# Kernel tuning notes

Hardware: AMD Instinct MI355X
Metric: run time of the kernel (lower is better)

Reference implementation:

```python
import jax, jax.numpy as jnp
from jax import lax
import numpy as np

HIDDEN_DIM = 64
INPUT_DIM = 1
NUM_CLASSES = 3
B, T = 2048, 512


def _lstm_layer(x_tbd, w_ih, w_hh, b_ih, b_hh):
    # x_tbd: [T, B, D_in]; PyTorch gate order: i, f, g, o
    H = w_hh.shape[1]
    bsz = x_tbd.shape[1]
    # precompute input projections for all timesteps: [T, B, 4H]
    xp = jnp.einsum('tbd,gd->tbg', x_tbd, w_ih) + b_ih + b_hh

    def step(carry, xg):
        h, c = carry
        gates = xg + h @ w_hh.T  # [B, 4H]
        i, f, g, o = jnp.split(gates, 4, axis=-1)
        i = jax.nn.sigmoid(i)
        f = jax.nn.sigmoid(f)
        g = jnp.tanh(g)
        o = jax.nn.sigmoid(o)
        c = f * c + i * g
        h = o * jnp.tanh(c)
        return (h, c), h

    h0 = jnp.zeros((bsz, H), dtype=x_tbd.dtype)
    c0 = jnp.zeros((bsz, H), dtype=x_tbd.dtype)
    (h_last, _), ys = lax.scan(step, (h0, c0), xp)
    return ys, h_last


def setup_inputs() -> dict:
    key = jax.random.key(0)
    ks = jax.random.split(key, 12)
    s_in = 1.0 / np.sqrt(HIDDEN_DIM)
    H4 = 4 * HIDDEN_DIM
    return {
        'x': jax.random.normal(ks[0], (B, T, INPUT_DIM), dtype=jnp.float32),
        'w_ih0': jax.random.uniform(ks[1], (H4, INPUT_DIM), minval=-s_in, maxval=s_in),
        'w_hh0': jax.random.uniform(ks[2], (H4, HIDDEN_DIM), minval=-s_in, maxval=s_in),
        'b_ih0': jax.random.uniform(ks[3], (H4,), minval=-s_in, maxval=s_in),
        'b_hh0': jax.random.uniform(ks[4], (H4,), minval=-s_in, maxval=s_in),
        'w_ih1': jax.random.uniform(ks[5], (H4, HIDDEN_DIM), minval=-s_in, maxval=s_in),
        'w_hh1': jax.random.uniform(ks[6], (H4, HIDDEN_DIM), minval=-s_in, maxval=s_in),
        'b_ih1': jax.random.uniform(ks[7], (H4,), minval=-s_in, maxval=s_in),
        'b_hh1': jax.random.uniform(ks[8], (H4,), minval=-s_in, maxval=s_in),
        'w_fc': jax.random.uniform(ks[9], (NUM_CLASSES, HIDDEN_DIM), minval=-s_in, maxval=s_in),
        'b_fc': jax.random.uniform(ks[10], (NUM_CLASSES,), minval=-s_in, maxval=s_in),
    }


def reference(x, w_ih0, w_hh0, b_ih0, b_hh0, w_ih1, w_hh1, b_ih1, b_hh1, w_fc, b_fc):
    # eval-mode forward (dropout between layers disabled)
    x_tbd = jnp.transpose(x, (1, 0, 2))  # [T, B, 1]
    ys0, _ = _lstm_layer(x_tbd, w_ih0, w_hh0, b_ih0, b_hh0)  # [T, B, H]
    _, h_last = _lstm_layer(ys0, w_ih1, w_hh1, b_ih1, b_hh1)  # [B, H]
    return h_last @ w_fc.T + b_fc  # [B, NUM_CLASSES]
```

## Files before the change

### kernel.cpp

```cpp
#include <hip/hip_runtime.h>


typedef _Float16 half8    __attribute__((ext_vector_type(8)));
typedef float    float4_t __attribute__((ext_vector_type(4)));
typedef float    float2_t __attribute__((ext_vector_type(2)));

#define T_STEPS 512
#define SIG_K  (-1.442695040888963f)
#define TANH_K (-2.885390081777927f)

__device__ __forceinline__ int hoff(int slot, int row, int kb, int lo) {
    return slot * 1024 + row * 64 + (((kb + row) & 7) << 3) + lo;
}

__device__ __forceinline__ float lstm_cell(float zi, float zf, float zg, float zo,
                                           float& c) {
    const float ei = __builtin_amdgcn_exp2f(zi);
    const float ef = __builtin_amdgcn_exp2f(zf);
    const float v  = __builtin_amdgcn_exp2f(zg);
    const float eo = __builtin_amdgcn_exp2f(zo);
    const float pi = 1.f + ei, pf = 1.f + ef, pv = 1.f + v, po = 1.f + eo;
    const float A   = pi * pv;
    const float num = fmaf(c, A, (1.f - v) * pf);
    const float cn  = num * __builtin_amdgcn_rcpf(pf * A);
    c = cn;
    const float u = __builtin_amdgcn_exp2f(cn * TANH_K);
    return (1.f - u) * __builtin_amdgcn_rcpf(po * (1.f + u));
}

extern "C" __global__ __launch_bounds__(512, 1)
void lstm2_mfma(const float* __restrict__ x,
                const float* __restrict__ w_ih0, const float* __restrict__ w_hh0,
                const float* __restrict__ b_ih0, const float* __restrict__ b_hh0,
                const float* __restrict__ w_ih1, const float* __restrict__ w_hh1,
                const float* __restrict__ b_ih1, const float* __restrict__ b_hh1,
                const float* __restrict__ w_fc,  const float* __restrict__ b_fc,
                float* __restrict__ out)
{
    __shared__ float    x_lds[T_STEPS][8];
    __shared__ _Float16 bufA[2 * 1024];
    __shared__ _Float16 bufB[2 * 1024];
    __shared__ float    hfin[8][68];

    const int tid  = threadIdx.x;
    const int wv   = tid >> 6;
    const int lane = tid & 63;
    const int cr   = lane & 15;
    const int kg   = lane >> 4;
    const int rb   = kg * 4;
    const int b0   = blockIdx.x * 8;
    const bool isL0 = (wv < 4);
    const int u    = wv & 3;
    const int ucol = u * 16 + cr;
    const int wkb  = 2 * u + (cr >> 3);

    for (int idx = tid; idx < 8 * T_STEPS; idx += 512) {
        const int r = idx >> 9, t = idx & (T_STEPS - 1);
        x_lds[t][r] = x[(long)(b0 + r) * T_STEPS + t];
    }
    for (int idx = tid; idx < 2 * 1024; idx += 512) {
        bufA[idx] = (_Float16)0.f;
        bufB[idx] = (_Float16)0.f;
    }

    half8 wf[4][4];
    float bias[4], wi0[4];
    #pragma unroll
    for (int g = 0; g < 4; ++g) {
        const float sc = (g == 2) ? TANH_K : SIG_K;
        const int col = g * 64 + ucol;
        if (isL0) {
            bias[g] = (b_ih0[col] + b_hh0[col]) * sc;
            wi0[g]  = w_ih0[col] * sc;
            #pragma unroll
            for (int kt = 0; kt < 2; ++kt) {
                const float* src = w_hh0 + col * 64 + kt * 32 + kg * 8;
                #pragma unroll
                for (int i = 0; i < 8; ++i) wf[g][kt][i] = (_Float16)(src[i] * sc);
            }
        } else {
            bias[g] = (b_ih1[col] + b_hh1[col]) * sc;
            #pragma unroll
            for (int kt = 0; kt < 4; ++kt) {
                const int k0 = kt * 32 + kg * 8;
                const float* src = (k0 < 64) ? (w_ih1 + col * 64 + k0)
                                             : (w_hh1 + col * 64 + (k0 - 64));
                #pragma unroll
                for (int i = 0; i < 8; ++i) wf[g][kt][i] = (_Float16)(src[i] * sc);
            }
        }
    }

    const float4_t zero4 = {0.f, 0.f, 0.f, 0.f};
    float cc[2] = {0.f, 0.f};
    float hv[2] = {0.f, 0.f};

    __syncthreads();

    for (int k = 0; k <= T_STEPS; ++k) {
        const int sA = (k + 1) & 1;

        if (isL0) {
            if (k < T_STEPS) {
                const half8 a0 = *(const half8*)&bufA[hoff(sA, cr, kg,     0)];
                const half8 a1 = *(const half8*)&bufA[hoff(sA, cr, 4 + kg, 0)];
                float4_t acc[4];
                #pragma unroll
                for (int g = 0; g < 4; ++g) {
                    acc[g] = __builtin_amdgcn_mfma_f32_16x16x32_f16(a0, wf[g][0], zero4, 0, 0, 0);
                    acc[g] = __builtin_amdgcn_mfma_f32_16x16x32_f16(a1, wf[g][1], acc[g], 0, 0, 0);
                }
                const float2_t xq = *(const float2_t*)&x_lds[k][2 * kg];
                #pragma unroll
                for (int ii = 0; ii < 2; ++ii) {
                    const float xv = xq[ii];
                    const float zi = fmaf(xv, wi0[0], acc[0][ii] + bias[0]);
                    const float zf = fmaf(xv, wi0[1], acc[1][ii] + bias[1]);
                    const float zg = fmaf(xv, wi0[2], acc[2][ii] + bias[2]);
                    const float zo = fmaf(xv, wi0[3], acc[3][ii] + bias[3]);
                    const float h = lstm_cell(zi, zf, zg, zo, cc[ii]);
                    bufA[hoff(k & 1, rb + ii, wkb, cr & 7)] = (_Float16)h;
                }
            }
        } else {
            if (k >= 1) {
                const int sB = k & 1;
                const half8 a0  = *(const half8*)&bufA[hoff(sA, cr, kg,     0)];
                const half8 a1  = *(const half8*)&bufA[hoff(sA, cr, 4 + kg, 0)];
                const half8 bh0 = *(const half8*)&bufB[hoff(sB, cr, kg,     0)];
                const half8 bh1 = *(const half8*)&bufB[hoff(sB, cr, 4 + kg, 0)];
                float4_t acc[4];
                #pragma unroll
                for (int g = 0; g < 4; ++g) {
                    acc[g] = __builtin_amdgcn_mfma_f32_16x16x32_f16(a0,  wf[g][0], zero4, 0, 0, 0);
                    acc[g] = __builtin_amdgcn_mfma_f32_16x16x32_f16(a1,  wf[g][1], acc[g], 0, 0, 0);
                    acc[g] = __builtin_amdgcn_mfma_f32_16x16x32_f16(bh0, wf[g][2], acc[g], 0, 0, 0);
                    acc[g] = __builtin_amdgcn_mfma_f32_16x16x32_f16(bh1, wf[g][3], acc[g], 0, 0, 0);
                }
                #pragma unroll
                for (int ii = 0; ii < 2; ++ii) {
                    const float zi = acc[0][ii] + bias[0];
                    const float zf = acc[1][ii] + bias[1];
                    const float zg = acc[2][ii] + bias[2];
                    const float zo = acc[3][ii] + bias[3];
                    hv[ii] = lstm_cell(zi, zf, zg, zo, cc[ii]);
                    bufB[hoff((k + 1) & 1, rb + ii, wkb, cr & 7)] = (_Float16)hv[ii];
                }
            }
        }

        __syncthreads();
    }

    if (!isL0) {
        hfin[2 * kg + 0][ucol] = hv[0];
        hfin[2 * kg + 1][ucol] = hv[1];
    }
    __syncthreads();

    if (tid < 24) {
        const int row = tid / 3, cls = tid - row * 3;
        float s = b_fc[cls];
        const float* wr = w_fc + cls * 64;
        #pragma unroll 8
        for (int uu = 0; uu < 64; ++uu) s += hfin[row][uu] * wr[uu];
        out[(long)(b0 + row) * 3 + cls] = s;
    }
}

extern "C" void kernel_launch(void* const* d_in, const int* in_sizes, int n_in,
                              void* d_out, int out_size, void* d_ws, size_t ws_size,
                              hipStream_t stream) {
    const float* xx     = (const float*)d_in[0];
    const float* w_ih0  = (const float*)d_in[1];
    const float* w_hh0  = (const float*)d_in[2];
    const float* b_ih0  = (const float*)d_in[3];
    const float* b_hh0  = (const float*)d_in[4];
    const float* w_ih1  = (const float*)d_in[5];
    const float* w_hh1  = (const float*)d_in[6];
    const float* b_ih1  = (const float*)d_in[7];
    const float* b_hh1  = (const float*)d_in[8];
    const float* w_fc   = (const float*)d_in[9];
    const float* b_fc   = (const float*)d_in[10];
    float* out = (float*)d_out;

    lstm2_mfma<<<dim3(256), dim3(512), 0, stream>>>(
        xx, w_ih0, w_hh0, b_ih0, b_hh0,
        w_ih1, w_hh1, b_ih1, b_hh1, w_fc, b_fc, out);
}
```

Measured before the change: 268.7 us.

## Halve batch rows per block and double grid to 512 blocks

Each block now processes 4 batch rows instead of 8, and the grid doubles to 512 blocks. Each lane computes one LSTM cell per step instead of two, which shortens the serial per-step critical path. Launch bounds are raised to allow up to 4 blocks per CU, so more blocks can share a CU and hide latency. The MFMA work per step is unchanged while half the output rows are discarded, so matrix-unit efficiency halves and total MFMA issue doubles.

```diff
diff --git a/kernel.cpp b/kernel.cpp
--- a/kernel.cpp
+++ b/kernel.cpp
@@ -3,7 +3,6 @@
 
 typedef _Float16 half8    __attribute__((ext_vector_type(8)));
 typedef float    float4_t __attribute__((ext_vector_type(4)));
-typedef float    float2_t __attribute__((ext_vector_type(2)));
 
 #define T_STEPS 512
 #define SIG_K  (-1.442695040888963f)
@@ -28,7 +27,7 @@
     return (1.f - u) * __builtin_amdgcn_rcpf(po * (1.f + u));
 }
 
-extern "C" __global__ __launch_bounds__(512, 1)
+extern "C" __global__ __launch_bounds__(512, 4)
 void lstm2_mfma(const float* __restrict__ x,
                 const float* __restrict__ w_ih0, const float* __restrict__ w_hh0,
                 const float* __restrict__ b_ih0, const float* __restrict__ b_hh0,
@@ -37,10 +36,10 @@
                 const float* __restrict__ w_fc,  const float* __restrict__ b_fc,
                 float* __restrict__ out)
 {
-    __shared__ float    x_lds[T_STEPS][8];
+    __shared__ float    x_lds[T_STEPS][4];
     __shared__ _Float16 bufA[2 * 1024];
     __shared__ _Float16 bufB[2 * 1024];
-    __shared__ float    hfin[8][68];
+    __shared__ float    hfin[4][68];
 
     const int tid  = threadIdx.x;
     const int wv   = tid >> 6;
@@ -48,13 +47,13 @@
     const int cr   = lane & 15;
     const int kg   = lane >> 4;
     const int rb   = kg * 4;
-    const int b0   = blockIdx.x * 8;
+    const int b0   = blockIdx.x * 4;
     const bool isL0 = (wv < 4);
     const int u    = wv & 3;
     const int ucol = u * 16 + cr;
     const int wkb  = 2 * u + (cr >> 3);
 
-    for (int idx = tid; idx < 8 * T_STEPS; idx += 512) {
+    for (int idx = tid; idx < 4 * T_STEPS; idx += 512) {
         const int r = idx >> 9, t = idx & (T_STEPS - 1);
         x_lds[t][r] = x[(long)(b0 + r) * T_STEPS + t];
     }
@@ -92,8 +91,8 @@
     }
 
     const float4_t zero4 = {0.f, 0.f, 0.f, 0.f};
-    float cc[2] = {0.f, 0.f};
-    float hv[2] = {0.f, 0.f};
+    float cc = 0.f;
+    float hv = 0.f;
 
     __syncthreads();
 
@@ -110,17 +109,13 @@
                     acc[g] = __builtin_amdgcn_mfma_f32_16x16x32_f16(a0, wf[g][0], zero4, 0, 0, 0);
                     acc[g] = __builtin_amdgcn_mfma_f32_16x16x32_f16(a1, wf[g][1], acc[g], 0, 0, 0);
                 }
-                const float2_t xq = *(const float2_t*)&x_lds[k][2 * kg];
-                #pragma unroll
-                for (int ii = 0; ii < 2; ++ii) {
-                    const float xv = xq[ii];
-                    const float zi = fmaf(xv, wi0[0], acc[0][ii] + bias[0]);
-                    const float zf = fmaf(xv, wi0[1], acc[1][ii] + bias[1]);
-                    const float zg = fmaf(xv, wi0[2], acc[2][ii] + bias[2]);
-                    const float zo = fmaf(xv, wi0[3], acc[3][ii] + bias[3]);
-                    const float h = lstm_cell(zi, zf, zg, zo, cc[ii]);
-                    bufA[hoff(k & 1, rb + ii, wkb, cr & 7)] = (_Float16)h;
-                }
+                const float xv = x_lds[k][kg];
+                const float zi = fmaf(xv, wi0[0], acc[0][0] + bias[0]);
+                const float zf = fmaf(xv, wi0[1], acc[1][0] + bias[1]);
+                const float zg = fmaf(xv, wi0[2], acc[2][0] + bias[2]);
+                const float zo = fmaf(xv, wi0[3], acc[3][0] + bias[3]);
+                const float h = lstm_cell(zi, zf, zg, zo, cc);
+                bufA[hoff(k & 1, rb, wkb, cr & 7)] = (_Float16)h;
             }
         } else {
             if (k >= 1) {
@@ -137,15 +132,12 @@
                     acc[g] = __builtin_amdgcn_mfma_f32_16x16x32_f16(bh0, wf[g][2], acc[g], 0, 0, 0);
                     acc[g] = __builtin_amdgcn_mfma_f32_16x16x32_f16(bh1, wf[g][3], acc[g], 0, 0, 0);
                 }
-                #pragma unroll
-                for (int ii = 0; ii < 2; ++ii) {
-                    const float zi = acc[0][ii] + bias[0];
-                    const float zf = acc[1][ii] + bias[1];
-                    const float zg = acc[2][ii] + bias[2];
-                    const float zo = acc[3][ii] + bias[3];
-                    hv[ii] = lstm_cell(zi, zf, zg, zo, cc[ii]);
-                    bufB[hoff((k + 1) & 1, rb + ii, wkb, cr & 7)] = (_Float16)hv[ii];
-                }
+                const float zi = acc[0][0] + bias[0];
+                const float zf = acc[1][0] + bias[1];
+                const float zg = acc[2][0] + bias[2];
+                const float zo = acc[3][0] + bias[3];
+                hv = lstm_cell(zi, zf, zg, zo, cc);
+                bufB[hoff((k + 1) & 1, rb, wkb, cr & 7)] = (_Float16)hv;
             }
         }
 
@@ -153,12 +145,11 @@
     }
 
     if (!isL0) {
-        hfin[2 * kg + 0][ucol] = hv[0];
-        hfin[2 * kg + 1][ucol] = hv[1];
+        hfin[kg][ucol] = hv;
     }
     __syncthreads();
 
-    if (tid < 24) {
+    if (tid < 12) {
         const int row = tid / 3, cls = tid - row * 3;
         float s = b_fc[cls];
         const float* wr = w_fc + cls * 64;
@@ -184,7 +175,7 @@
     const float* b_fc   = (const float*)d_in[10];
     float* out = (float*)d_out;
 
-    lstm2_mfma<<<dim3(256), dim3(512), 0, stream>>>(
+    lstm2_mfma<<<dim3(512), dim3(512), 0, stream>>>(
         xx, w_ih0, w_hh0, b_ih0, b_hh0,
         w_ih1, w_hh1, b_ih1, b_hh1, w_fc, b_fc, out);
 }
```

After: 275.9 us. 2.7% more time.
